# Kernel tuning notes

Hardware: AMD Instinct MI355X
Metric: run time of the kernel (lower is better)

Reference implementation:

```python
import jax, jax.numpy as jnp
import numpy as np

B, T, C, E = 4, 4096, 2048, 64

def setup_inputs() -> dict:
    key = jax.random.key(0)
    k1, k2 = jax.random.split(key)
    hidden_states = jax.random.normal(k1, (B, T, C), dtype=jnp.float32)
    sim_matrix = jax.random.normal(k2, (C, E), dtype=jnp.float32)
    gates = jnp.zeros((E,), dtype=jnp.float32)
    return {"hidden_states": hidden_states, "sim_matrix": sim_matrix, "gates": gates}

def reference(hidden_states, sim_matrix, gates):
    b, t, c = hidden_states.shape
    e = sim_matrix.shape[1]
    x = hidden_states.reshape(-1, c)                     # [N, C], N = B*T
    token_affinity = x @ sim_matrix                      # [N, E]
    logits = token_affinity - jax.nn.sigmoid(gates)      # [N, E]
    gated_logits = jax.nn.relu(logits)                   # [N, E]
    mask = (gated_logits > 0).astype(gated_logits.dtype) # STE forward
    inactive = jnp.sum(mask, axis=-1) == 0               # [N]
    fallback_count = jnp.sum(inactive).astype(jnp.float32)
    k_fallback = e // 2
    _, fb_idx = jax.lax.top_k(logits, k_fallback)        # [N, k]
    rows = jnp.arange(x.shape[0])[:, None]
    fb_mask = jnp.zeros_like(mask).at[rows, fb_idx].set(1.0)
    # inactive tokens have all-zero mask, so fallback simply replaces it
    activation_mask = jnp.where(inactive[:, None], fb_mask, mask)
    neg_max = jnp.finfo(gated_logits.dtype).min          # == -finfo.max
    masked = jnp.where(activation_mask > 0, gated_logits, neg_max)
    active_expert_probs = jax.nn.softmax(masked, axis=-1).reshape(b, t, e)
    return (active_expert_probs, fallback_count,
            logits.reshape(b, t, e), activation_mask.reshape(b, t, e))
```

## Files before the change

### kernel.cpp

```cpp
#include <hip/hip_runtime.h>
#include <hip/hip_bf16.h>

#define N_TOK   16384
#define C_DIM   2048
#define E_DIM   64
#define P_OFF   (N_TOK * E_DIM)
#define FB_OFF  P_OFF
#define LG_OFF  (P_OFF + 1)
#define AM_OFF  (2 * P_OFF + 1)

#define BPK_BYTES  262144
#define PART_BYTES ((size_t)4 * N_TOK * E_DIM * 2)

typedef __attribute__((ext_vector_type(8))) short bf16x8;
typedef __attribute__((ext_vector_type(4))) float f32x4;

static __device__ __forceinline__ unsigned short f2bf_rtn(float f) {
    unsigned u = __float_as_uint(f);
    unsigned r = u + 0x7FFFu + ((u >> 16) & 1u);
    return (unsigned short)(r >> 16);
}
static __device__ __forceinline__ float bf2f(unsigned short h) {
    return __uint_as_float(((unsigned)h) << 16);
}

__global__ void gating_prepack(const float* __restrict__ sim,
                               unsigned short* __restrict__ Bpk,
                               float* __restrict__ out) {
    int tid = blockIdx.x * 256 + threadIdx.x;
    if (tid == 0) out[FB_OFF] = 0.0f;
    if (tid >= C_DIM * E_DIM) return;
    int k = tid >> 6;
    int e = tid & 63;
    float v = sim[tid];
    int it = k >> 5;
    int gr = (k >> 3) & 3;
    int i  = k & 7;
    int lane = gr * 16 + (e & 15);
    int nb   = e >> 4;
    Bpk[it * 2048 + nb * 512 + lane * 8 + i] = f2bf_rtn(v);
}

__global__ __launch_bounds__(512, 4)
void gating_gemm(const float* __restrict__ x,
                 const unsigned short* __restrict__ Bpk,
                 unsigned short* __restrict__ part) {
    __shared__ unsigned short Blds[32768];

    const int tid = threadIdx.x;
    const int kq  = blockIdx.x & 3;
    const int tg  = blockIdx.x >> 2;

    const unsigned short* bq = Bpk + kq * 32768;
#pragma unroll
    for (int j = 0; j < 8; ++j) {
        __builtin_amdgcn_global_load_lds(
            (const __attribute__((address_space(1))) unsigned int*)(bq + j * 4096 + tid * 8),
            (__attribute__((address_space(3))) unsigned int*)(&Blds[j * 4096 + tid * 8]),
            16, 0, 0);
    }
    __syncthreads();

    const int l   = tid & 63;
    const int w   = tid >> 6;
    const int g   = l >> 4;
    const int e0  = l & 15;
    const int trow0 = tg * 128 + w * 16;
    const float* xr = x + (size_t)(trow0 + e0) * C_DIM + kq * 512 + g * 8;

    f32x4 acc[4];
#pragma unroll
    for (int nb = 0; nb < 4; ++nb) acc[nb] = (f32x4)0.0f;

    float4 Ac[4][2][2];
#pragma unroll
    for (int c = 0; c < 4; ++c)
#pragma unroll
        for (int st = 0; st < 2; ++st) {
            const float* ap = xr + (c * 2 + st) * 32;
            Ac[c][st][0] = *(const float4*)ap;
            Ac[c][st][1] = *(const float4*)(ap + 4);
        }

#pragma unroll
    for (int c = 0; c < 8; ++c) {
        const int sl = c & 3;

        float av[2][8];
#pragma unroll
        for (int st = 0; st < 2; ++st) {
            av[st][0] = Ac[sl][st][0].x; av[st][1] = Ac[sl][st][0].y;
            av[st][2] = Ac[sl][st][0].z; av[st][3] = Ac[sl][st][0].w;
            av[st][4] = Ac[sl][st][1].x; av[st][5] = Ac[sl][st][1].y;
            av[st][6] = Ac[sl][st][1].z; av[st][7] = Ac[sl][st][1].w;
        }

        if (c < 4) {
#pragma unroll
            for (int st = 0; st < 2; ++st) {
                const float* ap = xr + ((c + 4) * 2 + st) * 32;
                Ac[sl][st][0] = *(const float4*)ap;
                Ac[sl][st][1] = *(const float4*)(ap + 4);
            }
        }

#pragma unroll
        for (int st = 0; st < 2; ++st) {
            const int it = c * 2 + st;
            bf16x8 ah;
#pragma unroll
            for (int i = 0; i < 8; ++i) ah[i] = (short)f2bf_rtn(av[st][i]);
#pragma unroll
            for (int nb = 0; nb < 4; ++nb) {
                bf16x8 bf = *(const bf16x8*)(&Blds[it * 2048 + nb * 512 + l * 8]);
                acc[nb] = __builtin_amdgcn_mfma_f32_16x16x32_bf16(ah, bf, acc[nb], 0, 0, 0);
            }
        }
    }

    ushort4* pp = (ushort4*)part;
#pragma unroll
    for (int r = 0; r < 4; ++r) {
        int t = trow0 + g * 4 + r;
        ushort4 v;
        v.x = f2bf_rtn(acc[0][r]); v.y = f2bf_rtn(acc[1][r]);
        v.z = f2bf_rtn(acc[2][r]); v.w = f2bf_rtn(acc[3][r]);
        pp[(size_t)(kq * N_TOK + t) * 16 + e0] = v;
    }
}

__global__ __launch_bounds__(256, 4)
void gating_epi(const unsigned short* __restrict__ part,
                const float* __restrict__ gates,
                float* __restrict__ out) {
    const int tid = threadIdx.x;
    const int l   = tid & 63;
    const int w   = tid >> 6;
    const int g   = l >> 4;
    const int e0  = l & 15;
    const ushort4* pp = (const ushort4*)part;

    float sig[4];
#pragma unroll
    for (int nb = 0; nb < 4; ++nb)
        sig[nb] = 1.0f / (1.0f + expf(-gates[nb * 16 + e0]));

#pragma unroll
    for (int r = 0; r < 4; ++r) {
        const int t = blockIdx.x * 64 + w * 16 + g * 4 + r;
        float tot[4] = {0.0f, 0.0f, 0.0f, 0.0f};
#pragma unroll
        for (int s = 0; s < 4; ++s) {
            ushort4 v = pp[(size_t)(s * N_TOK + t) * 16 + e0];
            tot[0] += bf2f(v.x); tot[1] += bf2f(v.y);
            tot[2] += bf2f(v.z); tot[3] += bf2f(v.w);
        }
        float lg[4] = {tot[0] - sig[0], tot[1] - sig[1],
                       tot[2] - sig[2], tot[3] - sig[3]};
        bool  act[4];
        int   lcnt = 0;
        float lmax = -3.4e38f;
#pragma unroll
        for (int nb = 0; nb < 4; ++nb) {
            act[nb] = lg[nb] > 0.0f;
            if (act[nb]) { lcnt++; lmax = fmaxf(lmax, lg[nb]); }
        }
        int cnt = lcnt;
        float mx = lmax;
#pragma unroll
        for (int m = 1; m < 16; m <<= 1) {
            cnt += __shfl_xor(cnt, m, 16);
            mx   = fmaxf(mx, __shfl_xor(mx, m, 16));
        }

        float p[4], am[4];
        if (cnt > 0) {
            float ex[4], ls = 0.0f;
#pragma unroll
            for (int nb = 0; nb < 4; ++nb) {
                ex[nb] = act[nb] ? expf(lg[nb] - mx) : 0.0f;
                ls += ex[nb];
            }
            float Z = ls;
#pragma unroll
            for (int m = 1; m < 16; m <<= 1) Z += __shfl_xor(Z, m, 16);
            float rz = 1.0f / Z;
#pragma unroll
            for (int nb = 0; nb < 4; ++nb) {
                p[nb]  = ex[nb] * rz;
                am[nb] = act[nb] ? 1.0f : 0.0f;
            }
        } else {
            unsigned selm = 0;
            for (int it = 0; it < 32; ++it) {
                float bv = -3.4e38f;
                int   bi = 127;
#pragma unroll
                for (int nb = 0; nb < 4; ++nb) {
                    if (!((selm >> nb) & 1)) {
                        float v = lg[nb];
                        int   e = nb * 16 + e0;
                        if (v > bv || (v == bv && e < bi)) { bv = v; bi = e; }
                    }
                }
#pragma unroll
                for (int m = 1; m < 16; m <<= 1) {
                    float ov = __shfl_xor(bv, m, 16);
                    int   oi = __shfl_xor(bi, m, 16);
                    if (ov > bv || (ov == bv && oi < bi)) { bv = ov; bi = oi; }
                }
                if ((bi & 15) == e0) selm |= 1u << (bi >> 4);
            }
#pragma unroll
            for (int nb = 0; nb < 4; ++nb) {
                bool s_ = (selm >> nb) & 1;
                p[nb]  = s_ ? (1.0f / 32.0f) : 0.0f;
                am[nb] = s_ ? 1.0f : 0.0f;
            }
            if (e0 == 0) atomicAdd(&out[FB_OFF], 1.0f);
        }

#pragma unroll
        for (int nb = 0; nb < 4; ++nb) {
            int idx = t * 64 + nb * 16 + e0;
            out[idx]          = p[nb];
            out[LG_OFF + idx] = lg[nb];
            out[AM_OFF + idx] = am[nb];
        }
    }
}

__global__ __launch_bounds__(256, 4)
void gating_mono(const float* __restrict__ x,
                 const unsigned short* __restrict__ Bpk,
                 const float* __restrict__ gates,
                 float* __restrict__ out) {
    __shared__ float red[4][16][64];

    const int tid = threadIdx.x;
    const int l   = tid & 63;
    const int w   = tid >> 6;
    const int row0 = blockIdx.x * 16;
    const int g    = l >> 4;
    const int e0   = l & 15;
    const float* xr = x + (size_t)(row0 + e0) * C_DIM + w * 512 + g * 8;
    const unsigned short* bw = Bpk + (size_t)w * 16 * 2048 + l * 8;

    f32x4 acc[4];
#pragma unroll
    for (int nb = 0; nb < 4; ++nb) acc[nb] = (f32x4)0.0f;

    bf16x8 Bf[2][4];
#pragma unroll
    for (int b = 0; b < 2; ++b)
#pragma unroll
        for (int f = 0; f < 4; ++f)
            Bf[b][f] = *(const bf16x8*)(bw + b * 2048 + f * 512);
    float4 Ar[4][2];
#pragma unroll
    for (int it = 0; it < 4; ++it) {
        const float* ap = xr + it * 32;
        Ar[it][0] = *(const float4*)ap;
        Ar[it][1] = *(const float4*)(ap + 4);
    }

#pragma unroll
    for (int it = 0; it < 16; ++it) {
        const int sl = it & 3;
        const int bb = it & 1;
        bf16x8 bnx[4];
        if (it < 14) {
            const unsigned short* bp = bw + (it + 2) * 2048;
#pragma unroll
            for (int f = 0; f < 4; ++f) bnx[f] = *(const bf16x8*)(bp + f * 512);
        }
        float av[8] = {Ar[sl][0].x, Ar[sl][0].y, Ar[sl][0].z, Ar[sl][0].w,
                       Ar[sl][1].x, Ar[sl][1].y, Ar[sl][1].z, Ar[sl][1].w};
        if (it < 12) {
            const float* ap = xr + (it + 4) * 32;
            Ar[sl][0] = *(const float4*)ap;
            Ar[sl][1] = *(const float4*)(ap + 4);
        }
        bf16x8 ah;
#pragma unroll
        for (int i = 0; i < 8; ++i) ah[i] = (short)f2bf_rtn(av[i]);
#pragma unroll
        for (int nb = 0; nb < 4; ++nb)
            acc[nb] = __builtin_amdgcn_mfma_f32_16x16x32_bf16(ah, Bf[bb][nb], acc[nb], 0, 0, 0);
        if (it < 14) {
#pragma unroll
            for (int f = 0; f < 4; ++f) Bf[bb][f] = bnx[f];
        }
    }

#pragma unroll
    for (int nb = 0; nb < 4; ++nb)
#pragma unroll
        for (int r = 0; r < 4; ++r)
            red[w][nb * 4 + r][l] = acc[nb][r];
    __syncthreads();

    float tot[4];
#pragma unroll
    for (int nb = 0; nb < 4; ++nb)
        tot[nb] = red[0][nb * 4 + w][l] + red[1][nb * 4 + w][l]
                + red[2][nb * 4 + w][l] + red[3][nb * 4 + w][l];

    float sig[4];
#pragma unroll
    for (int nb = 0; nb < 4; ++nb)
        sig[nb] = 1.0f / (1.0f + expf(-gates[nb * 16 + e0]));

    const int t = row0 + g * 4 + w;
    float lg[4];
    bool  act[4];
    int   lcnt = 0;
    float lmax = -3.4e38f;
#pragma unroll
    for (int nb = 0; nb < 4; ++nb) {
        lg[nb]  = tot[nb] - sig[nb];
        act[nb] = lg[nb] > 0.0f;
        if (act[nb]) { lcnt++; lmax = fmaxf(lmax, lg[nb]); }
    }
    int cnt = lcnt;
    float mx = lmax;
#pragma unroll
    for (int m = 1; m < 16; m <<= 1) {
        cnt += __shfl_xor(cnt, m, 16);
        mx   = fmaxf(mx, __shfl_xor(mx, m, 16));
    }

    float p[4], am[4];
    if (cnt > 0) {
        float ex[4], ls = 0.0f;
#pragma unroll
        for (int nb = 0; nb < 4; ++nb) {
            ex[nb] = act[nb] ? expf(lg[nb] - mx) : 0.0f;
            ls += ex[nb];
        }
        float Z = ls;
#pragma unroll
        for (int m = 1; m < 16; m <<= 1) Z += __shfl_xor(Z, m, 16);
        float rz = 1.0f / Z;
#pragma unroll
        for (int nb = 0; nb < 4; ++nb) {
            p[nb]  = ex[nb] * rz;
            am[nb] = act[nb] ? 1.0f : 0.0f;
        }
    } else {
        unsigned selm = 0;
        for (int it = 0; it < 32; ++it) {
            float bv = -3.4e38f;
            int   bi = 127;
#pragma unroll
            for (int nb = 0; nb < 4; ++nb) {
                if (!((selm >> nb) & 1)) {
                    float v = lg[nb];
                    int   e = nb * 16 + e0;
                    if (v > bv || (v == bv && e < bi)) { bv = v; bi = e; }
                }
            }
#pragma unroll
            for (int m = 1; m < 16; m <<= 1) {
                float ov = __shfl_xor(bv, m, 16);
                int   oi = __shfl_xor(bi, m, 16);
                if (ov > bv || (ov == bv && oi < bi)) { bv = ov; bi = oi; }
            }
            if ((bi & 15) == e0) selm |= 1u << (bi >> 4);
        }
#pragma unroll
        for (int nb = 0; nb < 4; ++nb) {
            bool s_ = (selm >> nb) & 1;
            p[nb]  = s_ ? (1.0f / 32.0f) : 0.0f;
            am[nb] = s_ ? 1.0f : 0.0f;
        }
        if (e0 == 0) atomicAdd(&out[FB_OFF], 1.0f);
    }

#pragma unroll
    for (int nb = 0; nb < 4; ++nb) {
        int idx = t * 64 + nb * 16 + e0;
        out[idx]          = p[nb];
        out[LG_OFF + idx] = lg[nb];
        out[AM_OFF + idx] = am[nb];
    }
}

extern "C" void kernel_launch(void* const* d_in, const int* in_sizes, int n_in,
                              void* d_out, int out_size, void* d_ws, size_t ws_size,
                              hipStream_t stream) {
    const float* x     = (const float*)d_in[0];
    const float* sim   = (const float*)d_in[1];
    const float* gates = (const float*)d_in[2];
    float* out = (float*)d_out;
    unsigned short* Bpk = (unsigned short*)d_ws;

    gating_prepack<<<512, 256, 0, stream>>>(sim, Bpk, out);

    if (ws_size >= BPK_BYTES + PART_BYTES) {
        unsigned short* part = (unsigned short*)((char*)d_ws + BPK_BYTES);
        gating_gemm<<<512, 512, 0, stream>>>(x, Bpk, part);
        gating_epi<<<256, 256, 0, stream>>>(part, gates, out);
    } else {
        gating_mono<<<1024, 256, 0, stream>>>(x, Bpk, gates, out);
    }
}
```

Measured before the change: 40.53 us.

## Split K eight ways and stream A tiles through LDS with async global_load_lds

The GEMM kernel now splits the reduction dimension into 8 slices instead of 4 and launches twice as many blocks. The activation tile is staged through a per-wave triple-buffered, XOR-swizzled LDS ring filled by async global_load_lds, with explicit vmcnt waits replacing the register prefetch. The aim is more memory-level parallelism and better latency hiding on the streaming fp32 reads. In exchange, the partial-sum buffer doubles and the epilogue must read and sum 8 partials, and it relies on the workspace being large enough. It also switches float-to-bf16 conversion to the hardware intrinsic.

```diff
diff --git a/kernel.cpp b/kernel.cpp
--- a/kernel.cpp
+++ b/kernel.cpp
@@ -10,7 +10,7 @@
 #define AM_OFF  (2 * P_OFF + 1)
 
 #define BPK_BYTES  262144
-#define PART_BYTES ((size_t)4 * N_TOK * E_DIM * 2)
+#define PART_BYTES ((size_t)8 * N_TOK * E_DIM * 2)
 
 typedef __attribute__((ext_vector_type(8))) short bf16x8;
 typedef __attribute__((ext_vector_type(4))) float f32x4;
@@ -22,6 +22,10 @@
 }
 static __device__ __forceinline__ float bf2f(unsigned short h) {
     return __uint_as_float(((unsigned)h) << 16);
+}
+static __device__ __forceinline__ unsigned short f2bf_hw(float f) {
+    __hip_bfloat16 h = __float2bfloat16(f);
+    return *reinterpret_cast<unsigned short*>(&h);
 }
 
 __global__ void gating_prepack(const float* __restrict__ sim,
@@ -42,79 +46,83 @@
 }
 
 __global__ __launch_bounds__(512, 4)
-void gating_gemm(const float* __restrict__ x,
-                 const unsigned short* __restrict__ Bpk,
-                 unsigned short* __restrict__ part) {
-    __shared__ unsigned short Blds[32768];
+void gating_gemm8(const float* __restrict__ x,
+                  const unsigned short* __restrict__ Bpk,
+                  unsigned short* __restrict__ part) {
+    __shared__ __align__(16) unsigned short BldsU[16384];
+    __shared__ __align__(16) char Alds[49152];
 
     const int tid = threadIdx.x;
-    const int kq  = blockIdx.x & 3;
-    const int tg  = blockIdx.x >> 2;
-
-    const unsigned short* bq = Bpk + kq * 32768;
-#pragma unroll
-    for (int j = 0; j < 8; ++j) {
-        __builtin_amdgcn_global_load_lds(
-            (const __attribute__((address_space(1))) unsigned int*)(bq + j * 4096 + tid * 8),
-            (__attribute__((address_space(3))) unsigned int*)(&Blds[j * 4096 + tid * 8]),
-            16, 0, 0);
-    }
-    __syncthreads();
-
+    const int kq  = blockIdx.x & 7;
+    const int tg  = blockIdx.x >> 3;
     const int l   = tid & 63;
     const int w   = tid >> 6;
     const int g   = l >> 4;
     const int e0  = l & 15;
     const int trow0 = tg * 128 + w * 16;
-    const float* xr = x + (size_t)(trow0 + e0) * C_DIM + kq * 512 + g * 8;
+
+    const unsigned short* bq = Bpk + kq * 16384;
+#pragma unroll
+    for (int j = 0; j < 4; ++j) {
+        __builtin_amdgcn_global_load_lds(
+            (const __attribute__((address_space(1))) unsigned int*)(bq + j * 4096 + tid * 8),
+            (__attribute__((address_space(3))) unsigned int*)(&BldsU[j * 4096 + tid * 8]),
+            16, 0, 0);
+    }
+
+    const int rsub = l >> 3;
+    const int soff = ((((l & 7) * 16) ^ ((rsub & 3) << 5)) >> 2);
+    const float* xbase = x + (size_t)trow0 * C_DIM + kq * 256;
+    const float* src0 = xbase + (size_t)(0 + rsub) * C_DIM + soff;
+    const float* src1 = xbase + (size_t)(8 + rsub) * C_DIM + soff;
+    char* Aw = Alds + w * 6144;
+    const int dst_lane = l * 16;
+
+    auto issueA = [&](int i) {
+        char* d = Aw + (i % 3) * 2048;
+        __builtin_amdgcn_global_load_lds(
+            (const __attribute__((address_space(1))) unsigned int*)(src0 + i * 32),
+            (__attribute__((address_space(3))) unsigned int*)(d + dst_lane),
+            16, 0, 0);
+        __builtin_amdgcn_global_load_lds(
+            (const __attribute__((address_space(1))) unsigned int*)(src1 + i * 32),
+            (__attribute__((address_space(3))) unsigned int*)(d + 1024 + dst_lane),
+            16, 0, 0);
+    };
+
+    issueA(0);
+    issueA(1);
+    __syncthreads();
 
     f32x4 acc[4];
 #pragma unroll
     for (int nb = 0; nb < 4; ++nb) acc[nb] = (f32x4)0.0f;
 
-    float4 Ac[4][2][2];
-#pragma unroll
-    for (int c = 0; c < 4; ++c)
-#pragma unroll
-        for (int st = 0; st < 2; ++st) {
-            const float* ap = xr + (c * 2 + st) * 32;
-            Ac[c][st][0] = *(const float4*)ap;
-            Ac[c][st][1] = *(const float4*)(ap + 4);
-        }
-
-#pragma unroll
-    for (int c = 0; c < 8; ++c) {
-        const int sl = c & 3;
-
-        float av[2][8];
-#pragma unroll
-        for (int st = 0; st < 2; ++st) {
-            av[st][0] = Ac[sl][st][0].x; av[st][1] = Ac[sl][st][0].y;
-            av[st][2] = Ac[sl][st][0].z; av[st][3] = Ac[sl][st][0].w;
-            av[st][4] = Ac[sl][st][1].x; av[st][5] = Ac[sl][st][1].y;
-            av[st][6] = Ac[sl][st][1].z; av[st][7] = Ac[sl][st][1].w;
-        }
-
-        if (c < 4) {
-#pragma unroll
-            for (int st = 0; st < 2; ++st) {
-                const float* ap = xr + ((c + 4) * 2 + st) * 32;
-                Ac[sl][st][0] = *(const float4*)ap;
-                Ac[sl][st][1] = *(const float4*)(ap + 4);
-            }
-        }
-
-#pragma unroll
-        for (int st = 0; st < 2; ++st) {
-            const int it = c * 2 + st;
-            bf16x8 ah;
-#pragma unroll
-            for (int i = 0; i < 8; ++i) ah[i] = (short)f2bf_rtn(av[st][i]);
-#pragma unroll
-            for (int nb = 0; nb < 4; ++nb) {
-                bf16x8 bf = *(const bf16x8*)(&Blds[it * 2048 + nb * 512 + l * 8]);
-                acc[nb] = __builtin_amdgcn_mfma_f32_16x16x32_bf16(ah, bf, acc[nb], 0, 0, 0);
-            }
+    const int ardoff = e0 * 128 + ((g * 32) ^ ((e0 & 3) << 5));
+
+#pragma unroll
+    for (int i = 0; i < 8; ++i) {
+        if (i < 6) issueA(i + 2);
+        __builtin_amdgcn_sched_barrier(0);
+        if (i < 6)       asm volatile("s_waitcnt vmcnt(4)" ::: "memory");
+        else if (i == 6) asm volatile("s_waitcnt vmcnt(2)" ::: "memory");
+        else             asm volatile("s_waitcnt vmcnt(0)" ::: "memory");
+        __builtin_amdgcn_sched_barrier(0);
+
+        const char* ab = Aw + (i % 3) * 2048 + ardoff;
+        float4 a0 = *(const float4*)ab;
+        float4 a1 = *(const float4*)(ab + 16);
+        bf16x8 ah;
+        ah[0] = (short)f2bf_hw(a0.x); ah[1] = (short)f2bf_hw(a0.y);
+        ah[2] = (short)f2bf_hw(a0.z); ah[3] = (short)f2bf_hw(a0.w);
+        ah[4] = (short)f2bf_hw(a1.x); ah[5] = (short)f2bf_hw(a1.y);
+        ah[6] = (short)f2bf_hw(a1.z); ah[7] = (short)f2bf_hw(a1.w);
+
+        const unsigned short* bb = &BldsU[i * 2048 + l * 8];
+#pragma unroll
+        for (int nb = 0; nb < 4; ++nb) {
+            bf16x8 bf = *(const bf16x8*)(bb + nb * 512);
+            acc[nb] = __builtin_amdgcn_mfma_f32_16x16x32_bf16(ah, bf, acc[nb], 0, 0, 0);
         }
     }
 
@@ -125,7 +133,7 @@
         ushort4 v;
         v.x = f2bf_rtn(acc[0][r]); v.y = f2bf_rtn(acc[1][r]);
         v.z = f2bf_rtn(acc[2][r]); v.w = f2bf_rtn(acc[3][r]);
-        pp[(size_t)(kq * N_TOK + t) * 16 + e0] = v;
+        pp[((size_t)kq * N_TOK + t) * 16 + e0] = v;
     }
 }
 
@@ -150,8 +158,8 @@
         const int t = blockIdx.x * 64 + w * 16 + g * 4 + r;
         float tot[4] = {0.0f, 0.0f, 0.0f, 0.0f};
 #pragma unroll
-        for (int s = 0; s < 4; ++s) {
-            ushort4 v = pp[(size_t)(s * N_TOK + t) * 16 + e0];
+        for (int s = 0; s < 8; ++s) {
+            ushort4 v = pp[((size_t)s * N_TOK + t) * 16 + e0];
             tot[0] += bf2f(v.x); tot[1] += bf2f(v.y);
             tot[2] += bf2f(v.z); tot[3] += bf2f(v.w);
         }
@@ -283,7 +291,7 @@
         }
         bf16x8 ah;
 #pragma unroll
-        for (int i = 0; i < 8; ++i) ah[i] = (short)f2bf_rtn(av[i]);
+        for (int i = 0; i < 8; ++i) ah[i] = (short)f2bf_hw(av[i]);
 #pragma unroll
         for (int nb = 0; nb < 4; ++nb)
             acc[nb] = __builtin_amdgcn_mfma_f32_16x16x32_bf16(ah, Bf[bb][nb], acc[nb], 0, 0, 0);
@@ -399,7 +407,7 @@
 
     if (ws_size >= BPK_BYTES + PART_BYTES) {
         unsigned short* part = (unsigned short*)((char*)d_ws + BPK_BYTES);
-        gating_gemm<<<512, 512, 0, stream>>>(x, Bpk, part);
+        gating_gemm8<<<1024, 512, 0, stream>>>(x, Bpk, part);
         gating_epi<<<256, 256, 0, stream>>>(part, gates, out);
     } else {
         gating_mono<<<1024, 256, 0, stream>>>(x, Bpk, gates, out);
```

Result: slower. 42.57 us (+5.0%).
